# Kernel tuning notes

Measured on AMD Instinct MI355X. Metric: run time of the kernel, lower is better.

## Reference

```python
import jax, jax.numpy as jnp
import numpy as np
import math

B, S, F, D = 8, 2048, 1024, 1024
NEG = -1e9


def setup_inputs() -> dict:
    key = jax.random.key(0)
    ks = jax.random.split(key, 5)
    x = jax.random.normal(ks[0], (B, S, F), dtype=jnp.float32)
    r_mat = jax.random.normal(ks[1], (B, S, S), dtype=jnp.float32)
    # shared causal attention mask [S, S] (1 = keep, 0 = masked)
    attn_mask = jnp.tril(jnp.ones((S, S), dtype=jnp.float32))
    # per-batch padding mask [B, 1, S]: last 128 tokens of half the batch padded
    pad = jnp.ones((B, 1, S), dtype=jnp.float32)
    pad = pad.at[B // 2:, :, S - 128:].set(0.0)
    Wq = jax.random.normal(ks[2], (F, D), dtype=jnp.float32) / math.sqrt(F)
    Wk = jax.random.normal(ks[3], (F, D), dtype=jnp.float32) / math.sqrt(F)
    Wv = jax.random.normal(ks[4], (F, D), dtype=jnp.float32) / math.sqrt(F)
    return {"x": x, "r_mat": r_mat, "attn_mask": attn_mask, "pad_mask": pad,
            "Wq": Wq, "Wk": Wk, "Wv": Wv}


def reference(x, r_mat, attn_mask, pad_mask, Wq, Wk, Wv):
    scale = math.sqrt(x.shape[-1])  # original scales by sqrt(features)
    q = jnp.einsum('bsf,fd->bsd', x, Wq)
    k = jnp.einsum('bsf,fd->bsd', x, Wk)
    v = jnp.einsum('bsf,fd->bsd', x, Wv)
    scores = jnp.einsum('bsd,btd->bst', q, k) / scale  # [B, S, S]
    keep = (pad_mask != 0.0) & (attn_mask[None] != 0.0)  # [B, S, S] broadcast
    r = jnp.where(keep, r_mat, NEG)
    r = jax.nn.softmax(r, axis=-1)
    scores = jnp.where(keep, scores + r, NEG)
    prob = jax.nn.softmax(scores, axis=-1)
    return jnp.einsum('bst,btd->bsd', prob, v)
```

## Files before the change

kernel.cpp:

```cpp
#include <hip/hip_runtime.h>
#include <hip/hip_bf16.h>

#define B_ 8
#define S_ 2048
#define F_ 1024
#define D_ 1024

typedef unsigned short u16;
typedef float f32x4 __attribute__((ext_vector_type(4)));
typedef __bf16 bf16x8 __attribute__((ext_vector_type(8)));
typedef unsigned short u16x8 __attribute__((ext_vector_type(8)));

__device__ __forceinline__ u16 f2bf(float f) {
  union { float f; unsigned u; } v; v.f = f;
  unsigned r = v.u + 0x7fff + ((v.u >> 16) & 1);
  return (u16)(r >> 16);
}
__device__ __forceinline__ float bf2f(u16 b) {
  union { unsigned u; float f; } v; v.u = ((unsigned)b) << 16;
  return v.f;
}

__device__ __forceinline__ void stage16(const u16* g, u16* l) {
  __builtin_amdgcn_global_load_lds(
      (const __attribute__((address_space(1))) void*)g,
      (__attribute__((address_space(3))) void*)l, 16, 0, 0);
}


__global__ void cast_x(const float* __restrict__ x, u16* __restrict__ xb, int n4) {
  int i = blockIdx.x * blockDim.x + threadIdx.x;
  int stride = gridDim.x * blockDim.x;
  for (; i < n4; i += stride) {
    float4 v = ((const float4*)x)[i];
    ushort4 o;
    o.x = f2bf(v.x); o.y = f2bf(v.y); o.z = f2bf(v.z); o.w = f2bf(v.w);
    ((ushort4*)xb)[i] = o;
  }
}

__global__ void transW(const float* __restrict__ Wq, const float* __restrict__ Wk,
                       const float* __restrict__ Wv, u16* __restrict__ Wt) {
  __shared__ float tile[32][33];
  int z = blockIdx.z;
  const float* W = (z == 0) ? Wq : ((z == 1) ? Wk : Wv);
  int f0 = blockIdx.y * 32, d0 = blockIdx.x * 32;
  int tx = threadIdx.x & 31, ty = threadIdx.x >> 5;
  for (int i = 0; i < 4; i++)
    tile[ty + i * 8][tx] = W[(size_t)(f0 + ty + i * 8) * D_ + d0 + tx];
  __syncthreads();
  u16* o = Wt + (size_t)z * D_ * F_;
  for (int i = 0; i < 4; i++)
    o[(size_t)(d0 + ty + i * 8) * F_ + f0 + tx] = f2bf(tile[tx][ty + i * 8]);
}

__global__ __launch_bounds__(256) void r_rowsum(const float* __restrict__ r,
                                                const float* __restrict__ pm,
                                                float* __restrict__ rs) {
  int row = blockIdx.x;
  int b = row >> 11, s = row & 2047;
  const float4* rp = (const float4*)(r + (size_t)row * S_);
  const float4* pp = (const float4*)(pm + (size_t)b * S_);
  int nv = (s >> 2) + 1;
  float acc = 0.f;
  for (int i = threadIdx.x; i < nv; i += 256) {
    float4 rv = rp[i];
    float4 pv = pp[i];
    int t0 = i << 2;
    #pragma unroll
    for (int j = 0; j < 4; j++) {
      int t = t0 + j;
      if (t <= s && (&pv.x)[j] != 0.f) acc += __expf((&rv.x)[j] - 16.f);
    }
  }
  for (int off = 1; off < 64; off <<= 1) acc += __shfl_xor(acc, off);
  __shared__ float wsum[4];
  int lane = threadIdx.x & 63, w = threadIdx.x >> 6;
  if (lane == 0) wsum[w] = acc;
  __syncthreads();
  if (threadIdx.x == 0) rs[row] = wsum[0] + wsum[1] + wsum[2] + wsum[3];
}


__device__ __forceinline__ bf16x8 readfrag(const u16* lds, int row, int ks, int hi) {
  int c = ((ks << 6) + (hi << 4)) ^ ((row & 7) << 4);
  return *(const bf16x8*)((const char*)lds + row * 128 + c);
}

#define SYNC_POINT()                                                             \
  __builtin_amdgcn_sched_barrier(0);                                             \
  __builtin_amdgcn_s_barrier();                                                  \
  __builtin_amdgcn_sched_barrier(0);


__device__ __forceinline__ void stageA(const u16* __restrict__ src, int ld, int h,
                                       u16* ldsA, int w, int l) {
  int base = ((w >> 2) * 128) + h * 64 + ((w & 3) * 16);
  int r = l >> 3, ch = (l & 7) ^ (l >> 3);
  #pragma unroll
  for (int i = 0; i < 2; i++) {
    int row = base + i * 8;
    stage16(src + (size_t)(row + r) * ld + ch * 8, ldsA + row * 64);
  }
}
__device__ __forceinline__ void stageB(const u16* __restrict__ src, int ld, int h,
                                       u16* ldsB, int w, int l) {
  int base = h * 128 + w * 16;
  int r = l >> 3, ch = (l & 7) ^ (l >> 3);
  #pragma unroll
  for (int i = 0; i < 2; i++) {
    int row = base + i * 8;
    stage16(src + (size_t)(row + r) * ld + ch * 8, ldsB + row * 64);
  }
}

#define MFMA_QUAD(MB, KB)                                                        \
  __builtin_amdgcn_s_setprio(1);                                                 \
  _Pragma("unroll")                                                              \
  for (int m = 0; m < 4; m++)                                                    \
    _Pragma("unroll")                                                            \
    for (int n = 0; n < 4; n++)                                                  \
      acc[(MB) + m][n] = __builtin_amdgcn_mfma_f32_16x16x32_bf16(                \
          af[m], bfr[(KB) + n], acc[(MB) + m][n], 0, 0, 0);                      \
  __builtin_amdgcn_s_setprio(0);

__device__ __forceinline__ void gemm256(const u16* __restrict__ A, int lda,
                                        const u16* __restrict__ B, int ldb,
                                        int nT, u16* lds, f32x4 acc[8][4]) {
  const int t = threadIdx.x, w = t >> 6, l = t & 63;
  const int wr = w >> 2, wc = w & 3;
  u16* A0 = lds;           u16* B0 = lds + 16384;
  u16* A1 = lds + 32768;   u16* B1 = lds + 49152;

  #pragma unroll
  for (int m = 0; m < 8; m++)
    #pragma unroll
    for (int n = 0; n < 4; n++)
      #pragma unroll
      for (int j = 0; j < 4; j++) acc[m][n][j] = 0.f;

  stageB(B, ldb, 0, B0, w, l);
  stageB(B, ldb, 1, B0, w, l);
  stageA(A, lda, 0, A0, w, l);
  stageA(A, lda, 1, A0, w, l);
  if (nT > 1) stageA(A + 64, lda, 0, A1, w, l);
  asm volatile("s_waitcnt vmcnt(4)" ::: "memory");
  SYNC_POINT()

  const int arow = wr * 128 + (l & 15), brow = wc * 64 + (l & 15), hi = l >> 4;

  for (int kt = 0; kt < nT; kt++) {
    u16* cA = (kt & 1) ? A1 : A0;
    u16* cB = (kt & 1) ? B1 : B0;
    u16* nA = (kt & 1) ? A0 : A1;
    u16* nB = (kt & 1) ? B0 : B1;
    const u16* An1 = A + (size_t)(kt + 1) * 64;
    const u16* Bn1 = B + (size_t)(kt + 1) * 64;
    const u16* An2 = A + (size_t)(kt + 2) * 64;
    const bool has1 = (kt + 1 < nT), has2 = (kt + 2 < nT);
    bf16x8 af[4], bfr[8];

    #pragma unroll
    for (int m = 0; m < 4; m++) af[m] = readfrag(cA, arow + m * 16, 0, hi);
    #pragma unroll
    for (int n = 0; n < 4; n++) bfr[n] = readfrag(cB, brow + n * 16, 0, hi);
    if (has1) stageB(Bn1, ldb, 0, nB, w, l);
    MFMA_QUAD(0, 0)

    #pragma unroll
    for (int m = 0; m < 4; m++) af[m] = readfrag(cA, arow + m * 16, 1, hi);
    #pragma unroll
    for (int n = 0; n < 4; n++) bfr[4 + n] = readfrag(cB, brow + n * 16, 1, hi);
    if (has1) {
      stageB(Bn1, ldb, 1, nB, w, l);
      asm volatile("s_waitcnt vmcnt(4)" ::: "memory");
    } else {
      asm volatile("s_waitcnt vmcnt(0)" ::: "memory");
    }
    SYNC_POINT()
    MFMA_QUAD(0, 4)

    #pragma unroll
    for (int m = 0; m < 4; m++) af[m] = readfrag(cA, arow + 64 + m * 16, 0, hi);
    if (has2) stageA(An2, lda, 0, cA, w, l);
    MFMA_QUAD(4, 0)

    #pragma unroll
    for (int m = 0; m < 4; m++) af[m] = readfrag(cA, arow + 64 + m * 16, 1, hi);
    if (has1) stageA(An1, lda, 1, nA, w, l);
    if (has1 && has2)  { asm volatile("s_waitcnt vmcnt(4)" ::: "memory"); }
    else if (has1)     { asm volatile("s_waitcnt vmcnt(2)" ::: "memory"); }
    else               { asm volatile("s_waitcnt vmcnt(0)" ::: "memory"); }
    SYNC_POINT()
    MFMA_QUAD(4, 4)
  }
}

__device__ __forceinline__ void store256_bf16(f32x4 acc[8][4], u16* smem,
                                              u16* dst, int ld) {
  int t = threadIdx.x, w = t >> 6, l = t & 63;
  int wr = w >> 2, wc = w & 3;
  #pragma unroll
  for (int q = 0; q < 4; q++) {
    __syncthreads();
    if (wr == (q >> 1)) {
      int mb = (q & 1) * 4;
      #pragma unroll
      for (int mm = 0; mm < 4; mm++)
        #pragma unroll
        for (int j = 0; j < 4; j++) {
          int row = mm * 16 + (l >> 4) * 4 + j;
          #pragma unroll
          for (int n = 0; n < 4; n++)
            smem[row * 264 + wc * 64 + n * 16 + (l & 15)] = f2bf(acc[mb + mm][n][j]);
        }
    }
    __syncthreads();
    #pragma unroll
    for (int i = 0; i < 4; i++) {
      int idx = i * 512 + t;
      int row = idx >> 5, ch = idx & 31;
      *(u16x8*)(dst + (size_t)(q * 64 + row) * ld + ch * 8) =
          *(const u16x8*)(smem + row * 264 + ch * 8);
    }
  }
}

__global__ __launch_bounds__(512, 2) void gemm_qkv(
    const u16* __restrict__ xb, const u16* __restrict__ Wt,
    u16* __restrict__ qb, u16* __restrict__ kb, u16* __restrict__ vT) {
  __shared__ __align__(16) u16 lds[65536];
  int z = blockIdx.z;
  f32x4 acc[8][4];
  if (z < 2) {
    int m0 = blockIdx.x * 256, n0 = blockIdx.y * 256;
    gemm256(xb + (size_t)m0 * F_, F_,
            Wt + (size_t)z * D_ * F_ + (size_t)n0 * F_, F_, F_ / 64, lds, acc);
    store256_bf16(acc, lds, ((z == 0) ? qb : kb) + (size_t)m0 * D_ + n0, D_);
  } else {
    int d0 = blockIdx.y * 256, s0g = blockIdx.x * 256;
    gemm256(Wt + 2ULL * D_ * F_ + (size_t)d0 * F_, F_,
            xb + (size_t)s0g * F_, F_, F_ / 64, lds, acc);
    int b = s0g >> 11, s0 = s0g & 2047;
    store256_bf16(acc, lds, vT + (size_t)b * D_ * S_ + (size_t)d0 * S_ + s0, S_);
  }
}


__device__ __forceinline__ void stage128(const u16* __restrict__ src, int ld, int h,
                                         u16* ldsT, int w, int l) {
  int base = h * 64 + w * 16;
  int r = l >> 3, ch = (l & 7) ^ (l >> 3);
  #pragma unroll
  for (int i = 0; i < 2; i++) {
    int row = base + i * 8;
    stage16(src + (size_t)(row + r) * ld + ch * 8, ldsT + row * 64);
  }
}

#define MFMA16(AF, BF)                                                           \
  __builtin_amdgcn_s_setprio(1);                                                 \
  _Pragma("unroll")                                                              \
  for (int m = 0; m < 4; m++)                                                    \
    _Pragma("unroll")                                                            \
    for (int n = 0; n < 4; n++)                                                  \
      acc[m][n] = __builtin_amdgcn_mfma_f32_16x16x32_bf16(                       \
          AF[m], BF[n], acc[m][n], 0, 0, 0);                                     \
  __builtin_amdgcn_s_setprio(0);

__device__ __forceinline__ void gemm128(const u16* __restrict__ A, int lda,
                                        const u16* __restrict__ B, int ldb,
                                        int nT, u16* lds, f32x4 acc[4][4]) {
  const int t = threadIdx.x, w = t >> 6, l = t & 63;
  const int wr = w >> 1, wc = w & 1;
  u16* A0 = lds;          u16* B0 = lds + 8192;
  u16* A1 = lds + 16384;  u16* B1 = lds + 24576;

  #pragma unroll
  for (int m = 0; m < 4; m++)
    #pragma unroll
    for (int n = 0; n < 4; n++)
      #pragma unroll
      for (int j = 0; j < 4; j++) acc[m][n][j] = 0.f;

  stage128(A, lda, 0, A0, w, l);
  stage128(A, lda, 1, A0, w, l);
  stage128(B, ldb, 0, B0, w, l);
  stage128(B, ldb, 1, B0, w, l);
  if (nT > 1) {
    stage128(A + 64, lda, 0, A1, w, l);
    stage128(A + 64, lda, 1, A1, w, l);
    asm volatile("s_waitcnt vmcnt(4)" ::: "memory");
  } else {
    asm volatile("s_waitcnt vmcnt(0)" ::: "memory");
  }
  SYNC_POINT()

  const int arow = wr * 64 + (l & 15), brow = wc * 64 + (l & 15), hi = l >> 4;

  for (int kt = 0; kt < nT; kt++) {
    u16* cA = (kt & 1) ? A1 : A0;
    u16* cB = (kt & 1) ? B1 : B0;
    u16* nB = (kt & 1) ? B0 : B1;
    const bool has1 = (kt + 1 < nT), has2 = (kt + 2 < nT);
    bf16x8 a0f[4], b0f[4], a1f[4], b1f[4];

    #pragma unroll
    for (int m = 0; m < 4; m++) a0f[m] = readfrag(cA, arow + m * 16, 0, hi);
    #pragma unroll
    for (int n = 0; n < 4; n++) b0f[n] = readfrag(cB, brow + n * 16, 0, hi);
    #pragma unroll
    for (int m = 0; m < 4; m++) a1f[m] = readfrag(cA, arow + m * 16, 1, hi);
    #pragma unroll
    for (int n = 0; n < 4; n++) b1f[n] = readfrag(cB, brow + n * 16, 1, hi);
    if (has1) {
      stage128(B + (size_t)(kt + 1) * 64, ldb, 0, nB, w, l);
      stage128(B + (size_t)(kt + 1) * 64, ldb, 1, nB, w, l);
    }
    MFMA16(a0f, b0f)
    asm volatile("s_waitcnt lgkmcnt(0)" ::: "memory");
    SYNC_POINT()

    if (has2) {
      stage128(A + (size_t)(kt + 2) * 64, lda, 0, cA, w, l);
      stage128(A + (size_t)(kt + 2) * 64, lda, 1, cA, w, l);
    }
    MFMA16(a1f, b1f)
    if (has2)      { asm volatile("s_waitcnt vmcnt(4)" ::: "memory"); }
    else if (has1) { asm volatile("s_waitcnt vmcnt(0)" ::: "memory"); }
    SYNC_POINT()
  }
}

__global__ __launch_bounds__(256, 2) void attn_scores(
    const u16* __restrict__ qb, const u16* __restrict__ kb,
    const float* __restrict__ r_mat, const float* __restrict__ pm,
    const float* __restrict__ rs_r, u16* __restrict__ P,
    float* __restrict__ rowsum) {
  __shared__ __align__(16) u16 lds[32768];
  int b = blockIdx.y;
  int x = blockIdx.x;
  int mt = (int)((sqrtf(8.f * x + 1.f) - 1.f) * 0.5f);
  while ((mt + 1) * (mt + 2) / 2 <= x) mt++;
  while (mt * (mt + 1) / 2 > x) mt--;
  int nt = x - mt * (mt + 1) / 2;
  int m0 = mt * 128, n0 = nt * 128;
  f32x4 acc[4][4];
  gemm128(qb + ((size_t)b * S_ + m0) * D_, D_,
          kb + ((size_t)b * S_ + n0) * D_, D_, D_ / 64, lds, acc);
  int t = threadIdx.x, w = t >> 6, l = t & 63;
  int wr = w >> 1, wc = w & 1;
  float* fs = (float*)lds;
  const float* rb = r_mat + (size_t)b * S_ * S_;
  const float* pmp = pm + (size_t)b * S_ + n0;
  #pragma unroll
  for (int h = 0; h < 2; h++) {
    __syncthreads();
    if (wr == h) {
      #pragma unroll
      for (int m = 0; m < 4; m++)
        #pragma unroll
        for (int j = 0; j < 4; j++) {
          int row = m * 16 + (l >> 4) * 4 + j;
          #pragma unroll
          for (int n = 0; n < 4; n++)
            fs[row * 132 + wc * 64 + n * 16 + (l & 15)] = acc[m][n][j];
        }
    }
    __syncthreads();
    int row = t >> 2, cg = t & 3;
    int srow = m0 + h * 64 + row;
    float invr = 1.f / rs_r[b * S_ + srow];
    const float* rrow = rb + (size_t)srow * S_ + n0 + cg * 32;
    u16* prow = P + (size_t)b * S_ * S_ + (size_t)srow * S_ + n0 + cg * 32;
    const float* fsc = fs + row * 132 + cg * 32;
    float rsum = 0.f;
    #pragma unroll
    for (int cc = 0; cc < 4; cc++) {
      int ch = (cg + cc) & 3;
      f32x4 q0 = *(const f32x4*)(fsc + ch * 8);
      f32x4 q1 = *(const f32x4*)(fsc + ch * 8 + 4);
      f32x4 r0 = *(const f32x4*)(rrow + ch * 8);
      f32x4 r1 = *(const f32x4*)(rrow + ch * 8 + 4);
      f32x4 p0 = *(const f32x4*)(pmp + cg * 32 + ch * 8);
      f32x4 p1 = *(const f32x4*)(pmp + cg * 32 + ch * 8 + 4);
      u16x8 o;
      #pragma unroll
      for (int k = 0; k < 8; k++) {
        int tc = n0 + cg * 32 + ch * 8 + k;
        float rv = (k < 4) ? r0[k] : r1[k - 4];
        float pmv = (k < 4) ? p0[k] : p1[k - 4];
        float qk = (k < 4) ? q0[k] : q1[k - 4];
        bool keep = (tc <= srow) && (pmv != 0.f);
        float rsm = __expf(rv - 16.f) * invr;
        float e = keep ? __expf(fmaf(qk, 0.03125f, rsm - 16.f)) : 0.f;
        u16 pb = f2bf(e); o[k] = pb; rsum += bf2f(pb);
      }
      *(u16x8*)(prow + ch * 8) = o;
    }
    rsum += __shfl_xor(rsum, 1);
    rsum += __shfl_xor(rsum, 2);
    if ((t & 3) == 0) atomicAdd(&rowsum[b * S_ + srow], rsum);
  }
}

__global__ __launch_bounds__(256, 2) void attn_pv(
    const u16* __restrict__ P, const u16* __restrict__ vT,
    const float* __restrict__ rowsum, float* __restrict__ out) {
  __shared__ __align__(16) u16 lds[32768];
  int mt = 15 - blockIdx.x, dt = blockIdx.y, b = blockIdx.z;
  int m0 = mt * 128, n0 = dt * 128;
  int nT = (m0 + 128) / 64;
  f32x4 acc[4][4];
  gemm128(P + ((size_t)b * S_ + m0) * S_, S_,
          vT + ((size_t)b * D_ + n0) * S_, S_, nT, lds, acc);
  int t = threadIdx.x, w = t >> 6, l = t & 63;
  int wr = w >> 1, wc = w & 1;
  float* fs = (float*)lds;
  #pragma unroll
  for (int h = 0; h < 2; h++) {
    __syncthreads();
    if (wr == h) {
      #pragma unroll
      for (int m = 0; m < 4; m++)
        #pragma unroll
        for (int j = 0; j < 4; j++) {
          int row = m * 16 + (l >> 4) * 4 + j;
          float inv = 1.f / rowsum[b * S_ + m0 + h * 64 + row];
          #pragma unroll
          for (int n = 0; n < 4; n++)
            fs[row * 132 + wc * 64 + n * 16 + (l & 15)] = acc[m][n][j] * inv;
        }
    }
    __syncthreads();
    #pragma unroll
    for (int i = 0; i < 8; i++) {
      int idx = i * 256 + t;
      int row = idx >> 5, c4 = (idx & 31) << 2;
      *(float4*)(out + ((size_t)b * S_ + m0 + h * 64 + row) * D_ + n0 + c4) =
          *(const float4*)(fs + row * 132 + c4);
    }
  }
}

extern "C" void kernel_launch(void* const* d_in, const int* in_sizes, int n_in,
                              void* d_out, int out_size, void* d_ws, size_t ws_size,
                              hipStream_t stream) {
  const float* x     = (const float*)d_in[0];
  const float* r_mat = (const float*)d_in[1];
  const float* pm    = (const float*)d_in[3];
  const float* Wq    = (const float*)d_in[4];
  const float* Wk    = (const float*)d_in[5];
  const float* Wv    = (const float*)d_in[6];
  float* out = (float*)d_out;
  char* ws = (char*)d_ws;

  u16*   qb     = (u16*)(ws + 0);
  u16*   kb     = (u16*)(ws + 33554432ULL);
  u16*   vT     = (u16*)(ws + 67108864ULL);
  float* rs_r   = (float*)(ws + 100663296ULL);
  float* rowsum = (float*)(ws + 100728832ULL);
  u16*   P      = (u16*)(ws + 100794368ULL);
  u16*   xb     = (u16*)(ws + 100794368ULL);
  u16*   Wt     = (u16*)(ws + 134348800ULL);

  cast_x<<<dim3(2048), dim3(256), 0, stream>>>(x, xb, (B_ * S_ * F_) / 4);
  transW<<<dim3(32, 32, 3), dim3(256), 0, stream>>>(Wq, Wk, Wv, Wt);
  r_rowsum<<<dim3(B_ * S_), dim3(256), 0, stream>>>(r_mat, pm, rs_r);
  gemm_qkv<<<dim3(64, 4, 3), dim3(512), 0, stream>>>(xb, Wt, qb, kb, vT);
  hipMemsetAsync(rowsum, 0, B_ * S_ * sizeof(float), stream);
  attn_scores<<<dim3(136, 8), dim3(256), 0, stream>>>(qb, kb, r_mat, pm, rs_r, P, rowsum);
  attn_pv<<<dim3(16, 8, 8), dim3(256), 0, stream>>>(P, vT, rowsum, out);
}
```

Measured before the change: 307.3 us.

## Swizzle block IDs across XCDs and load both k-halves of A fragments upfront

```diff
diff --git a/kernel.cpp b/kernel.cpp
--- a/kernel.cpp
+++ b/kernel.cpp
@@ -25,6 +25,11 @@
   __builtin_amdgcn_global_load_lds(
       (const __attribute__((address_space(1))) void*)g,
       (__attribute__((address_space(3))) void*)l, 16, 0, 0);
+}
+
+__device__ __forceinline__ int xcd_swz(int f, int n) {
+  int per = n >> 3;
+  return (f & 7) * per + (f >> 3);
 }
 
 
@@ -114,14 +119,14 @@
   }
 }
 
-#define MFMA_QUAD(MB, KB)                                                        \
+#define MFMAQ(AF, KB, MB)                                                        \
   __builtin_amdgcn_s_setprio(1);                                                 \
   _Pragma("unroll")                                                              \
   for (int m = 0; m < 4; m++)                                                    \
     _Pragma("unroll")                                                            \
     for (int n = 0; n < 4; n++)                                                  \
       acc[(MB) + m][n] = __builtin_amdgcn_mfma_f32_16x16x32_bf16(                \
-          af[m], bfr[(KB) + n], acc[(MB) + m][n], 0, 0, 0);                      \
+          AF[m], bfr[(KB) + n], acc[(MB) + m][n], 0, 0, 0);                      \
   __builtin_amdgcn_s_setprio(0);
 
 __device__ __forceinline__ void gemm256(const u16* __restrict__ A, int lda,
@@ -158,19 +163,19 @@
     const u16* Bn1 = B + (size_t)(kt + 1) * 64;
     const u16* An2 = A + (size_t)(kt + 2) * 64;
     const bool has1 = (kt + 1 < nT), has2 = (kt + 2 < nT);
-    bf16x8 af[4], bfr[8];
-
-    #pragma unroll
-    for (int m = 0; m < 4; m++) af[m] = readfrag(cA, arow + m * 16, 0, hi);
+    bf16x8 af0[4], af1[4], bfr[8];
+
+    #pragma unroll
+    for (int m = 0; m < 4; m++) af0[m] = readfrag(cA, arow + m * 16, 0, hi);
     #pragma unroll
     for (int n = 0; n < 4; n++) bfr[n] = readfrag(cB, brow + n * 16, 0, hi);
+    #pragma unroll
+    for (int m = 0; m < 4; m++) af1[m] = readfrag(cA, arow + m * 16, 1, hi);
+    #pragma unroll
+    for (int n = 0; n < 4; n++) bfr[4 + n] = readfrag(cB, brow + n * 16, 1, hi);
     if (has1) stageB(Bn1, ldb, 0, nB, w, l);
-    MFMA_QUAD(0, 0)
-
-    #pragma unroll
-    for (int m = 0; m < 4; m++) af[m] = readfrag(cA, arow + m * 16, 1, hi);
-    #pragma unroll
-    for (int n = 0; n < 4; n++) bfr[4 + n] = readfrag(cB, brow + n * 16, 1, hi);
+    MFMAQ(af0, 0, 0)
+
     if (has1) {
       stageB(Bn1, ldb, 1, nB, w, l);
       asm volatile("s_waitcnt vmcnt(4)" ::: "memory");
@@ -178,21 +183,21 @@
       asm volatile("s_waitcnt vmcnt(0)" ::: "memory");
     }
     SYNC_POINT()
-    MFMA_QUAD(0, 4)
-
-    #pragma unroll
-    for (int m = 0; m < 4; m++) af[m] = readfrag(cA, arow + 64 + m * 16, 0, hi);
+    MFMAQ(af1, 4, 0)
+
+    #pragma unroll
+    for (int m = 0; m < 4; m++) af0[m] = readfrag(cA, arow + 64 + m * 16, 0, hi);
+    #pragma unroll
+    for (int m = 0; m < 4; m++) af1[m] = readfrag(cA, arow + 64 + m * 16, 1, hi);
     if (has2) stageA(An2, lda, 0, cA, w, l);
-    MFMA_QUAD(4, 0)
-
-    #pragma unroll
-    for (int m = 0; m < 4; m++) af[m] = readfrag(cA, arow + 64 + m * 16, 1, hi);
+    MFMAQ(af0, 0, 4)
+
     if (has1) stageA(An1, lda, 1, nA, w, l);
     if (has1 && has2)  { asm volatile("s_waitcnt vmcnt(4)" ::: "memory"); }
     else if (has1)     { asm volatile("s_waitcnt vmcnt(2)" ::: "memory"); }
     else               { asm volatile("s_waitcnt vmcnt(0)" ::: "memory"); }
     SYNC_POINT()
-    MFMA_QUAD(4, 4)
+    MFMAQ(af1, 4, 4)
   }
 }
 
@@ -230,15 +235,16 @@
     const u16* __restrict__ xb, const u16* __restrict__ Wt,
     u16* __restrict__ qb, u16* __restrict__ kb, u16* __restrict__ vT) {
   __shared__ __align__(16) u16 lds[65536];
-  int z = blockIdx.z;
+  int f = xcd_swz(blockIdx.x + 64 * blockIdx.y + 256 * blockIdx.z, 768);
+  int bx = f & 63, by = (f >> 6) & 3, z = f >> 8;
   f32x4 acc[8][4];
   if (z < 2) {
-    int m0 = blockIdx.x * 256, n0 = blockIdx.y * 256;
+    int m0 = bx * 256, n0 = by * 256;
     gemm256(xb + (size_t)m0 * F_, F_,
             Wt + (size_t)z * D_ * F_ + (size_t)n0 * F_, F_, F_ / 64, lds, acc);
     store256_bf16(acc, lds, ((z == 0) ? qb : kb) + (size_t)m0 * D_ + n0, D_);
   } else {
-    int d0 = blockIdx.y * 256, s0g = blockIdx.x * 256;
+    int d0 = by * 256, s0g = bx * 256;
     gemm256(Wt + 2ULL * D_ * F_ + (size_t)d0 * F_, F_,
             xb + (size_t)s0g * F_, F_, F_ / 64, lds, acc);
     int b = s0g >> 11, s0 = s0g & 2047;
@@ -338,8 +344,8 @@
     const float* __restrict__ rs_r, u16* __restrict__ P,
     float* __restrict__ rowsum) {
   __shared__ __align__(16) u16 lds[32768];
-  int b = blockIdx.y;
-  int x = blockIdx.x;
+  int f = xcd_swz(blockIdx.x + 136 * blockIdx.y, 1088);
+  int x = f % 136, b = f / 136;
   int mt = (int)((sqrtf(8.f * x + 1.f) - 1.f) * 0.5f);
   while ((mt + 1) * (mt + 2) / 2 <= x) mt++;
   while (mt * (mt + 1) / 2 > x) mt--;
@@ -408,7 +414,8 @@
     const u16* __restrict__ P, const u16* __restrict__ vT,
     const float* __restrict__ rowsum, float* __restrict__ out) {
   __shared__ __align__(16) u16 lds[32768];
-  int mt = 15 - blockIdx.x, dt = blockIdx.y, b = blockIdx.z;
+  int f = xcd_swz(blockIdx.x + 16 * blockIdx.y + 128 * blockIdx.z, 1024);
+  int mt = 15 - (f & 15), dt = (f >> 4) & 7, b = f >> 7;
   int m0 = mt * 128, n0 = dt * 128;
   int nT = (m0 + 128) / 64;
   f32x4 acc[4][4];
```

After: 280.8 us. 1.09x faster.
